# Optimization experiments

Hardware: AMD Instinct MI355X
Metric: run time of the kernel (lower is better)

The kernel has to match this reference:

```python
import jax, jax.numpy as jnp
import numpy as np

L, D, H, HD = 2, 2048, 16, 128          # layers, hidden, heads, head_dim
E, K, F, FS = 8, 2, 1408, 5632           # experts, top_k, moe_inter, shared_inter
V, T = 32000, 2048                       # vocab, tokens
EPS = 1e-6
ROPE_BASE = 1000000.0


def _rms(x, w):
    return x * jax.lax.rsqrt(jnp.mean(x * x, axis=-1, keepdims=True) + EPS) * w


def _rope(x, cos, sin):
    half = x.shape[-1] // 2
    x1, x2 = x[..., :half], x[..., half:]
    return jnp.concatenate([x1 * cos - x2 * sin, x1 * sin + x2 * cos], axis=-1)


def setup_inputs() -> dict:
    key = jax.random.key(0)
    ks = jax.random.split(key, 18)
    s = 0.02
    f = lambda k, shp: jax.random.normal(k, shp, jnp.float32) * s
    return {
        "input_ids": jax.random.randint(ks[0], (T,), 0, V, dtype=jnp.int32),
        "positions": jnp.arange(T, dtype=jnp.int32),
        "embed": f(ks[1], (V, D)),
        "qw": f(ks[2], (L, D, H * HD)),
        "kw": f(ks[3], (L, D, H * HD)),
        "vw": f(ks[4], (L, D, H * HD)),
        "ow": f(ks[5], (L, H * HD, D)),
        "ln1": jnp.ones((L, D), jnp.float32),
        "ln2": jnp.ones((L, D), jnp.float32),
        "router_w": f(ks[6], (L, D, E)),
        "sgate_w": f(ks[7], (L, D)),
        "wg": f(ks[8], (L, E, D, F)),
        "wu": f(ks[9], (L, E, D, F)),
        "wd": f(ks[10], (L, E, F, D)),
        "swg": f(ks[11], (L, D, FS)),
        "swu": f(ks[12], (L, D, FS)),
        "swd": f(ks[13], (L, FS, D)),
        "final_ln": jnp.ones((D,), jnp.float32),
    }


def _attn(x, positions, qw_l, kw_l, vw_l, ow_l):
    q = (x @ qw_l).reshape(T, H, HD)
    k = (x @ kw_l).reshape(T, H, HD)
    v = (x @ vw_l).reshape(T, H, HD)
    half = HD // 2
    inv = 1.0 / (ROPE_BASE ** (jnp.arange(half, dtype=jnp.float32) / half))
    ang = positions.astype(jnp.float32)[:, None] * inv[None, :]  # [T, half]
    cos, sin = jnp.cos(ang)[:, None, :], jnp.sin(ang)[:, None, :]
    q = _rope(q, cos, sin)
    k = _rope(k, cos, sin)
    scores = jnp.einsum('thd,shd->hts', q, k) * (HD ** -0.5)  # [H, T, T]
    mask = positions[:, None] >= positions[None, :]  # causal
    scores = jnp.where(mask[None], scores, -1e30)
    p = jax.nn.softmax(scores, axis=-1)
    o = jnp.einsum('hts,shd->thd', p, v).reshape(T, H * HD)
    return o @ ow_l


def _moe(x, router_w_l, sgate_w_l, wg_l, wu_l, wd_l, swg_l, swu_l, swd_l):
    # shared expert + its sigmoid gate
    sh = (jax.nn.silu(x @ swg_l) * (x @ swu_l)) @ swd_l
    sgate = jax.nn.sigmoid(x @ sgate_w_l)[:, None]
    # router: softmax in float32, then top-k with prob renorm (norm_topk_prob)
    probs = jax.nn.softmax((x @ router_w_l).astype(jnp.float32), axis=-1)
    topv, topi = jax.lax.top_k(probs, K)
    topv = topv / jnp.sum(topv, axis=-1, keepdims=True)
    combine = jnp.sum(jax.nn.one_hot(topi, E, dtype=x.dtype) * topv[..., None].astype(x.dtype), axis=1)  # [T, E]
    # dense grouped expert FFN, combined by routing weights (scatter-add equivalent)
    g = jnp.einsum('td,edf->etf', x, wg_l)
    u = jnp.einsum('td,edf->etf', x, wu_l)
    y = jnp.einsum('etf,efd->etd', jax.nn.silu(g) * u, wd_l)
    moe_out = jnp.einsum('te,etd->td', combine, y)
    return (moe_out + sgate * sh) * (1.0 / K ** 0.5)


def reference(input_ids, positions, embed, qw, kw, vw, ow, ln1, ln2, router_w,
              sgate_w, wg, wu, wd, swg, swu, swd, final_ln):
    h = embed[input_ids]  # [T, D]
    residual = None
    for l in range(L):
        if residual is None:
            residual = h
            x = _rms(h, ln1[l])
        else:
            residual = h + residual
            x = _rms(residual, ln1[l])
        h = _attn(x, positions, qw[l], kw[l], vw[l], ow[l])
        residual = h + residual
        x = _rms(residual, ln2[l])
        h = _moe(x, router_w[l], sgate_w[l], wg[l], wu[l], wd[l], swg[l], swu[l], swd[l])
    residual = h + residual
    return _rms(residual, final_ln)
```

## Files before the change

### kernel.cpp

```cpp
#include <hip/hip_runtime.h>
#include <stdint.h>

#define TT 2048
#define DD 2048
#define HH 16
#define HDIM 128
#define NE 8
#define TOPK 2
#define FF 1408
#define FSS 5632
#define NL 2

typedef __bf16 bf16;
typedef __bf16 bf16x2 __attribute__((ext_vector_type(2)));
typedef __bf16 bf16x4 __attribute__((ext_vector_type(4)));
typedef __bf16 bf16x8 __attribute__((ext_vector_type(8)));
typedef float f32x4 __attribute__((ext_vector_type(4)));

__device__ __forceinline__ void split1(float f, bf16& h, bf16& l) {
  bf16 hb = (bf16)f;
  h = hb;
  l = (bf16)(f - (float)hb);
}

__device__ __forceinline__ void gload16(const void* g, void* l) {
  __builtin_amdgcn_global_load_lds((const __attribute__((address_space(1))) void*)g,
                                   (__attribute__((address_space(3))) void*)l, 16, 0, 0);
}

template<bool LO>
__launch_bounds__(256)
__global__ void k_wtrans(const float* __restrict__ W, bf16* __restrict__ Wh,
                         bf16* __restrict__ Wl, int Kd, int N)
{
  __shared__ float T[64][68];
  const size_t slab = (size_t)blockIdx.z * (size_t)Kd * (size_t)N;
  const float* Wp = W + slab;
  const int k0 = blockIdx.x * 64, n0 = blockIdx.y * 64;
  const int tid = threadIdx.x;
  const int rr = tid >> 2, c4 = (tid & 3) * 4;
  const float* src = Wp + (size_t)(k0 + rr) * N + n0 + c4;
#pragma unroll
  for (int j = 0; j < 4; ++j) {
    f32x4 v = *(const f32x4*)(src + j * 16);
    *(f32x4*)&T[rr][c4 + j * 16] = v;
  }
  __syncthreads();
  const int nn = tid >> 2, kk = (tid & 3) * 16;
  bf16x8 h0, h1, l0, l1;
#pragma unroll
  for (int j = 0; j < 8; ++j) {
    bf16 hb, lb;
    split1(T[kk + j][nn], hb, lb);
    h0[j] = hb; l0[j] = lb;
    split1(T[kk + 8 + j][nn], hb, lb);
    h1[j] = hb; l1[j] = lb;
  }
  size_t out = slab + (size_t)(n0 + nn) * Kd + k0 + kk;
  *(bf16x8*)&Wh[out] = h0;
  *(bf16x8*)&Wh[out + 8] = h1;
  if (LO) {
    *(bf16x8*)&Wl[out] = l0;
    *(bf16x8*)&Wl[out + 8] = l1;
  }
}

template<int BMT, int NT, bool EXPERT, bool GATHER, int OM>
__launch_bounds__(256, (BMT == 128 ? 3 : 4))
__global__ void k_gemmp(const bf16* __restrict__ Ah, const bf16* __restrict__ Al,
                        const bf16* __restrict__ Bh, const bf16* __restrict__ Bl,
                        void* __restrict__ C1, void* __restrict__ C2,
                        int M, int N, int Kd, int lda, int ldc,
                        const int* __restrict__ perm, const int* __restrict__ cnt,
                        const int* __restrict__ ofs)
{
  constexpr int PL = (NT == 3) ? 2 : 1;
  constexpr int ASUB = BMT / 16;
  constexpr int AISS = PL * ASUB;
  constexpr int BISS = PL * 8;
  constexpr int QPW = (AISS + BISS) / 4;
  constexpr int IF = BMT / 32;

  int m_count = M, row_base = 0;
  size_t boff = 0;
  if (EXPERT) {
    int e = blockIdx.z;
    m_count = cnt[e];
    if ((int)(blockIdx.x * BMT) >= m_count) return;
    row_base = ofs[e];
    boff = (size_t)e * (size_t)N * (size_t)Kd;
  }
  const int tid = threadIdx.x, lane = tid & 63, wid = tid >> 6;
  const int wm = (wid >> 1) * (BMT / 2), wn = (wid & 1) * 64;
  const int lr = lane & 15, g = lane >> 4;
  const int n0 = blockIdx.y * 128;
  const int m0 = blockIdx.x * BMT;

  __shared__ bf16 As[PL][BMT][32];
  __shared__ bf16 Bs[PL][128][32];

  const bf16* srcp[QPW];
#pragma unroll
  for (int j = 0; j < QPW; ++j) {
    int q = wid * QPW + j;
    int r16 = lane >> 2;
    int kc = (lane & 3) ^ ((lane >> 3) & 3);
    if (q < AISS) {
      int pl = q / ASUB, sub = q % ASUB;
      int r = sub * 16 + r16;
      int tok;
      if (EXPERT) {
        int lrow = m0 + r;
        if (lrow >= m_count) lrow = m_count - 1;
        tok = GATHER ? perm[row_base + lrow] : (row_base + lrow);
      } else {
        tok = m0 + r;
      }
      const bf16* base = (pl == 0) ? Ah : Al;
      srcp[j] = base + (size_t)tok * lda + kc * 8;
    } else {
      int qb = q - AISS;
      int pl = qb >> 3, sub = qb & 7;
      int nrow = sub * 16 + r16;
      const bf16* base = (pl == 0) ? Bh : Bl;
      srcp[j] = base + boff + (size_t)(n0 + nrow) * Kd + kc * 8;
    }
  }

  f32x4 acc[IF][4];
#pragma unroll
  for (int i = 0; i < IF; ++i)
#pragma unroll
    for (int j = 0; j < 4; ++j)
      acc[i][j] = (f32x4){0.f, 0.f, 0.f, 0.f};

  auto ISSUE = [&](int k0) {
#pragma unroll
    for (int j = 0; j < QPW; ++j) {
      int q = wid * QPW + j;
      bf16* dst;
      if (q < AISS) {
        int pl = q / ASUB, sub = q % ASUB;
        dst = &As[pl][sub * 16][0];
      } else {
        int qb = q - AISS;
        int pl = qb >> 3, sub = qb & 7;
        dst = &Bs[pl][sub * 16][0];
      }
      gload16(srcp[j] + k0, dst);
    }
  };

  const int gs = (g ^ ((lr >> 1) & 3)) * 8;
  const int NTk = Kd >> 5;
  ISSUE(0);
  for (int t = 0; t < NTk; ++t) {
    __syncthreads();
    bf16x8 bfr[4][PL], afr[IF][PL];
#pragma unroll
    for (int jj = 0; jj < 4; ++jj)
#pragma unroll
      for (int pl = 0; pl < PL; ++pl)
        bfr[jj][pl] = *(const bf16x8*)&Bs[pl][wn + jj * 16 + lr][gs];
#pragma unroll
    for (int i = 0; i < IF; ++i)
#pragma unroll
      for (int pl = 0; pl < PL; ++pl)
        afr[i][pl] = *(const bf16x8*)&As[pl][wm + i * 16 + lr][gs];
    __syncthreads();
    if (t + 1 < NTk) ISSUE((t + 1) << 5);
#pragma unroll
    for (int i = 0; i < IF; ++i)
#pragma unroll
      for (int jj = 0; jj < 4; ++jj) {
        f32x4 a2 = acc[i][jj];
        a2 = __builtin_amdgcn_mfma_f32_16x16x32_bf16(afr[i][0], bfr[jj][0], a2, 0, 0, 0);
        if (NT == 3) {
          a2 = __builtin_amdgcn_mfma_f32_16x16x32_bf16(afr[i][0], bfr[jj][1], a2, 0, 0, 0);
          a2 = __builtin_amdgcn_mfma_f32_16x16x32_bf16(afr[i][1], bfr[jj][0], a2, 0, 0, 0);
        }
        acc[i][jj] = a2;
      }
  }

  const int r0 = g * 4;
#pragma unroll
  for (int i = 0; i < IF; ++i) {
    int lrow0 = m0 + wm + i * 16 + r0;
#pragma unroll
    for (int j = 0; j < 4; ++j) {
      int col = n0 + wn + j * 16 + lr;
      if (OM == 4) {
        bf16x4 ph, pl;
#pragma unroll
        for (int r = 0; r < 4; ++r) { bf16 hb, lb; split1(acc[i][j][r], hb, lb); ph[r] = hb; pl[r] = lb; }
        *(bf16x4*)&((bf16*)C1)[(size_t)col * ldc + lrow0] = ph;
        *(bf16x4*)&((bf16*)C2)[(size_t)col * ldc + lrow0] = pl;
      } else {
#pragma unroll
        for (int r = 0; r < 4; ++r) {
          int lrow = lrow0 + r;
          if (EXPERT && lrow >= m_count) continue;
          size_t off = (size_t)(row_base + lrow) * ldc + col;
          if (OM == 1) {
            ((float*)C1)[off] = acc[i][j][r];
          } else {
            bf16 hb, lb; split1(acc[i][j][r], hb, lb);
            ((bf16*)C1)[off] = hb;
            ((bf16*)C2)[off] = lb;
          }
        }
      }
    }
  }
}

__launch_bounds__(256)
__global__ void k_attns(const bf16* __restrict__ Qh, const bf16* __restrict__ Ql,
                        const bf16* __restrict__ Kh, const bf16* __restrict__ Kl,
                        const bf16* __restrict__ Vh, const bf16* __restrict__ Vl,
                        bf16* __restrict__ Oh, bf16* __restrict__ Ol)
{
  const int tid = threadIdx.x;
  const int lane = tid & 63, wid = tid >> 6;
  const int head = blockIdx.y;
  const int qbase = (gridDim.x - 1 - blockIdx.x) * 16;
  const int lr = lane & 15, g = lane >> 4;

  __shared__ float o_l[4][16][132];
  __shared__ float m_l[4][16], l_l[4][16];
  bf16* plbase = (bf16*)&o_l[0][0][0];
  bf16 (*pl_h)[40] = (bf16(*)[40])(plbase + wid * 16 * 40);
  bf16 (*pl_l)[40] = (bf16(*)[40])(plbase + (4 + wid) * 16 * 40);

  bf16x8 qfh[4], qfl[4];
  {
    size_t qoff = (size_t)(qbase + lr) * DD + head * HDIM;
#pragma unroll
    for (int c = 0; c < 4; ++c) {
      qfh[c] = *(const bf16x8*)(Qh + qoff + c * 32 + g * 8);
      qfl[c] = *(const bf16x8*)(Ql + qoff + c * 32 + g * 8);
    }
  }

  f32x4 o[8];
#pragma unroll
  for (int d = 0; d < 8; ++d) o[d] = (f32x4){0.f, 0.f, 0.f, 0.f};
  float m_r = -1e30f, l_r = 0.f;

  const int qend = qbase + 16;
  for (int kb = wid * 32; kb < qend; kb += 128) {
    f32x4 s0 = {0.f,0.f,0.f,0.f}, s1 = {0.f,0.f,0.f,0.f};
    size_t k0off = (size_t)(kb + lr) * DD + head * HDIM;
    size_t k1off = k0off + (size_t)16 * DD;
#pragma unroll
    for (int c = 0; c < 4; ++c) {
      bf16x8 kh = *(const bf16x8*)(Kh + k0off + c * 32 + g * 8);
      bf16x8 kl = *(const bf16x8*)(Kl + k0off + c * 32 + g * 8);
      s0 = __builtin_amdgcn_mfma_f32_16x16x32_bf16(kh, qfh[c], s0, 0, 0, 0);
      s0 = __builtin_amdgcn_mfma_f32_16x16x32_bf16(kl, qfh[c], s0, 0, 0, 0);
      s0 = __builtin_amdgcn_mfma_f32_16x16x32_bf16(kh, qfl[c], s0, 0, 0, 0);
    }
#pragma unroll
    for (int c = 0; c < 4; ++c) {
      bf16x8 kh = *(const bf16x8*)(Kh + k1off + c * 32 + g * 8);
      bf16x8 kl = *(const bf16x8*)(Kl + k1off + c * 32 + g * 8);
      s1 = __builtin_amdgcn_mfma_f32_16x16x32_bf16(kh, qfh[c], s1, 0, 0, 0);
      s1 = __builtin_amdgcn_mfma_f32_16x16x32_bf16(kl, qfh[c], s1, 0, 0, 0);
      s1 = __builtin_amdgcn_mfma_f32_16x16x32_bf16(kh, qfl[c], s1, 0, 0, 0);
    }
    float p0[4], p1[4];
    float mloc = -1e30f;
    const int q = qbase + lr;
#pragma unroll
    for (int r = 0; r < 4; ++r) {
      int k0i = kb + g * 4 + r;
      float a0 = s0[r] * 0.08838834764831845f;
      float a1 = s1[r] * 0.08838834764831845f;
      if (k0i > q)      a0 = -1e30f;
      if (k0i + 16 > q) a1 = -1e30f;
      p0[r] = a0; p1[r] = a1;
      mloc = fmaxf(mloc, fmaxf(a0, a1));
    }
    mloc = fmaxf(mloc, __shfl_xor(mloc, 16, 64));
    mloc = fmaxf(mloc, __shfl_xor(mloc, 32, 64));
    float mn = fmaxf(m_r, mloc);
    float alpha = __expf(m_r - mn);
    m_r = mn;
    float ps = 0.f;
#pragma unroll
    for (int r = 0; r < 4; ++r) {
      p0[r] = __expf(p0[r] - mn);
      p1[r] = __expf(p1[r] - mn);
      ps += p0[r] + p1[r];
    }
    ps += __shfl_xor(ps, 16, 64);
    ps += __shfl_xor(ps, 32, 64);
    l_r = l_r * alpha + ps;
    float alr[4];
#pragma unroll
    for (int r = 0; r < 4; ++r) alr[r] = __shfl(alpha, g * 4 + r, 64);
#pragma unroll
    for (int d = 0; d < 8; ++d)
#pragma unroll
      for (int r = 0; r < 4; ++r) o[d][r] *= alr[r];
#pragma unroll
    for (int r = 0; r < 4; ++r) {
      bf16 hb, lb;
      split1(p0[r], hb, lb);
      pl_h[lr][g * 4 + r] = hb;
      pl_l[lr][g * 4 + r] = lb;
      split1(p1[r], hb, lb);
      pl_h[lr][16 + g * 4 + r] = hb;
      pl_l[lr][16 + g * 4 + r] = lb;
    }
    bf16x8 pah = *(const bf16x8*)&pl_h[lr][g * 8];
    bf16x8 pal = *(const bf16x8*)&pl_l[lr][g * 8];
#pragma unroll
    for (int d = 0; d < 8; ++d) {
      size_t voff = (size_t)(head * HDIM + d * 16 + lr) * TT + kb + g * 8;
      bf16x8 vfh = *(const bf16x8*)(Vh + voff);
      bf16x8 vfl = *(const bf16x8*)(Vl + voff);
      o[d] = __builtin_amdgcn_mfma_f32_16x16x32_bf16(pah, vfh, o[d], 0, 0, 0);
      o[d] = __builtin_amdgcn_mfma_f32_16x16x32_bf16(pah, vfl, o[d], 0, 0, 0);
      o[d] = __builtin_amdgcn_mfma_f32_16x16x32_bf16(pal, vfh, o[d], 0, 0, 0);
    }
  }

  __syncthreads();
  if (g == 0) {
    m_l[wid][lr] = m_r;
    l_l[wid][lr] = l_r;
  }
#pragma unroll
  for (int d = 0; d < 8; ++d)
#pragma unroll
    for (int r = 0; r < 4; ++r)
      o_l[wid][g * 4 + r][d * 16 + lr] = o[d][r];
  __syncthreads();

  const int row = tid >> 4;
  const int c0 = (tid & 15) * 8;
  float m0v = m_l[0][row], m1v = m_l[1][row], m2v = m_l[2][row], m3v = m_l[3][row];
  float ms = fmaxf(fmaxf(m0v, m1v), fmaxf(m2v, m3v));
  float s0v = __expf(m0v - ms), s1v = __expf(m1v - ms);
  float s2v = __expf(m2v - ms), s3v = __expf(m3v - ms);
  float lsum = l_l[0][row] * s0v + l_l[1][row] * s1v
             + l_l[2][row] * s2v + l_l[3][row] * s3v;
  float inv = 1.f / lsum;
  union { bf16 b[8]; uint4 u; } ph, pl;
#pragma unroll
  for (int j = 0; j < 8; ++j) {
    float v = o_l[0][row][c0 + j] * s0v + o_l[1][row][c0 + j] * s1v
            + o_l[2][row][c0 + j] * s2v + o_l[3][row][c0 + j] * s3v;
    bf16 hb, lb;
    split1(v * inv, hb, lb);
    ph.b[j] = hb; pl.b[j] = lb;
  }
  size_t oi = (size_t)(qbase + row) * DD + head * HDIM + c0;
  *(uint4*)(Oh + oi) = ph.u;
  *(uint4*)(Ol + oi) = pl.u;
}

__global__ void k_embed(const int* __restrict__ ids, const float* __restrict__ Em,
                        float* __restrict__ Hout)
{
  int t = blockIdx.x, tid = threadIdx.x;
  const float4* s = (const float4*)(Em + (size_t)ids[t] * DD);
  float4* dst = (float4*)(Hout + (size_t)t * DD);
  dst[tid] = s[tid];
  dst[tid + 256] = s[tid + 256];
}

template<bool ADDIN, bool WF32, bool FINAL>
__launch_bounds__(256)
__global__ void k_addrms(const float* __restrict__ Hin, float* __restrict__ Res,
                         const float* __restrict__ W,
                         bf16* __restrict__ Xh, bf16* __restrict__ Xl,
                         float* __restrict__ Xf)
{
  const int t = blockIdx.x, tid = threadIdx.x;
  const size_t base = (size_t)t * DD + tid * 8;
  float x[8];
  {
    const float4* hp = (const float4*)(Hin + base);
    float4 a = hp[0], b = hp[1];
    x[0]=a.x; x[1]=a.y; x[2]=a.z; x[3]=a.w;
    x[4]=b.x; x[5]=b.y; x[6]=b.z; x[7]=b.w;
    if (ADDIN) {
      const float4* rp = (const float4*)(Res + base);
      float4 c = rp[0], d = rp[1];
      x[0]+=c.x; x[1]+=c.y; x[2]+=c.z; x[3]+=c.w;
      x[4]+=d.x; x[5]+=d.y; x[6]+=d.z; x[7]+=d.w;
    }
  }
  {
    float4* rp = (float4*)(Res + base);
    rp[0] = make_float4(x[0], x[1], x[2], x[3]);
    rp[1] = make_float4(x[4], x[5], x[6], x[7]);
  }
  float ss = 0.f;
#pragma unroll
  for (int j = 0; j < 8; ++j) ss += x[j] * x[j];
#pragma unroll
  for (int off = 32; off; off >>= 1) ss += __shfl_xor(ss, off, 64);
  __shared__ float red[4];
  if ((tid & 63) == 0) red[tid >> 6] = ss;
  __syncthreads();
  float tot = red[0] + red[1] + red[2] + red[3];
  float sc = rsqrtf(tot * (1.0f / DD) + 1e-6f);
  float y[8];
#pragma unroll
  for (int j = 0; j < 8; ++j) y[j] = x[j] * sc * W[tid * 8 + j];
  if (!FINAL) {
    union { bf16 b[8]; uint4 u; } ph, pl;
#pragma unroll
    for (int j = 0; j < 8; ++j) { bf16 hb, lb; split1(y[j], hb, lb); ph.b[j] = hb; pl.b[j] = lb; }
    *(uint4*)(Xh + base) = ph.u;
    *(uint4*)(Xl + base) = pl.u;
  }
  if (WF32 || FINAL) {
    float4* xp = (float4*)(Xf + base);
    xp[0] = make_float4(y[0], y[1], y[2], y[3]);
    xp[1] = make_float4(y[4], y[5], y[6], y[7]);
  }
}

__global__ void k_rope2(bf16* __restrict__ Qh, bf16* __restrict__ Ql,
                        bf16* __restrict__ Kh, bf16* __restrict__ Kl,
                        const int* __restrict__ pos)
{
  int idx = blockIdx.x * 256 + threadIdx.x;
  int d = idx & 63;
  int h = (idx >> 6) & (HH - 1);
  int t = idx >> 10;
  if (t >= TT) return;
  double inv = pow(1.0e6, -(double)d / 64.0);
  double ang = (double)pos[t] * inv;
  double sd, cd;
  sincos(ang, &sd, &cd);
  float sn = (float)sd, cs = (float)cd;
  size_t base = (size_t)t * DD + h * HDIM + d;
  float q1 = (float)Qh[base] + (float)Ql[base];
  float q2 = (float)Qh[base + 64] + (float)Ql[base + 64];
  float qa = q1 * cs - q2 * sn, qb = q1 * sn + q2 * cs;
  bf16 hb, lb;
  split1(qa, hb, lb); Qh[base] = hb;      Ql[base] = lb;
  split1(qb, hb, lb); Qh[base + 64] = hb; Ql[base + 64] = lb;
  float k1 = (float)Kh[base] + (float)Kl[base];
  float k2 = (float)Kh[base + 64] + (float)Kl[base + 64];
  float ka = k1 * cs - k2 * sn, kb2 = k1 * sn + k2 * cs;
  split1(ka, hb, lb);  Kh[base] = hb;      Kl[base] = lb;
  split1(kb2, hb, lb); Kh[base + 64] = hb; Kl[base + 64] = lb;
}

__launch_bounds__(64)
__global__ void k_router(const float* __restrict__ Xf, const float* __restrict__ RW,
                         const float* __restrict__ SGW, int* __restrict__ eidx,
                         float* __restrict__ ew, float* __restrict__ sgate,
                         int* __restrict__ cnt)
{
  const int t = blockIdx.x, lane = threadIdx.x;
  const float* x = Xf + (size_t)t * DD;
  float acc[8] = {0,0,0,0,0,0,0,0};
  float sg = 0.f;
  for (int i = lane; i < DD; i += 64) {
    float xv = x[i];
    const float4* w = (const float4*)(RW + (size_t)i * NE);
    float4 w0 = w[0], w1 = w[1];
    acc[0] += xv * w0.x; acc[1] += xv * w0.y; acc[2] += xv * w0.z; acc[3] += xv * w0.w;
    acc[4] += xv * w1.x; acc[5] += xv * w1.y; acc[6] += xv * w1.z; acc[7] += xv * w1.w;
    sg += xv * SGW[i];
  }
#pragma unroll
  for (int off = 32; off; off >>= 1) {
#pragma unroll
    for (int e = 0; e < 8; ++e) acc[e] += __shfl_xor(acc[e], off, 64);
    sg += __shfl_xor(sg, off, 64);
  }
  if (lane == 0) {
    int i0 = 0; float v0 = acc[0];
    for (int e = 1; e < 8; ++e) if (acc[e] > v0) { v0 = acc[e]; i0 = e; }
    int i1 = -1; float v1 = -1e30f;
    for (int e = 0; e < 8; ++e) if (e != i0 && acc[e] > v1) { v1 = acc[e]; i1 = e; }
    float w0 = 1.f / (1.f + expf(v1 - v0));
    eidx[2*t] = i0; eidx[2*t+1] = i1;
    ew[2*t] = w0; ew[2*t+1] = 1.f - w0;
    sgate[t] = 1.f / (1.f + expf(-sg));
    atomicAdd(&cnt[i0], 1);
    atomicAdd(&cnt[i1], 1);
  }
}

__global__ void k_scan(const int* __restrict__ cnt, int* __restrict__ ofs)
{
  if (threadIdx.x == 0) {
    int s = 0;
    for (int e = 0; e < NE; ++e) { ofs[e] = s; s += cnt[e]; }
    ofs[NE] = s;
  }
}

__global__ void k_assign(const int* __restrict__ eidx, const int* __restrict__ ofs,
                         int* __restrict__ cursor, int* __restrict__ perm,
                         int* __restrict__ posof)
{
  int t = blockIdx.x * 256 + threadIdx.x;
  if (t >= TT) return;
#pragma unroll
  for (int j = 0; j < 2; ++j) {
    int e = eidx[2*t + j];
    int p = ofs[e] + atomicAdd(&cursor[e], 1);
    perm[p] = t;
    posof[2*t + j] = p;
  }
}

__global__ void k_silup(const float* __restrict__ G, const float* __restrict__ U,
                        bf16* __restrict__ H, bf16* __restrict__ L)
{
  int i = (blockIdx.x * 256 + threadIdx.x) * 4;
  float4 g = *(const float4*)(G + i);
  float4 u = *(const float4*)(U + i);
  float s[4];
  s[0] = g.x / (1.f + expf(-g.x)) * u.x;
  s[1] = g.y / (1.f + expf(-g.y)) * u.y;
  s[2] = g.z / (1.f + expf(-g.z)) * u.z;
  s[3] = g.w / (1.f + expf(-g.w)) * u.w;
  bf16x4 h, l;
#pragma unroll
  for (int j = 0; j < 4; ++j) { bf16 hb, lb; split1(s[j], hb, lb); h[j] = hb; l[j] = lb; }
  *(bf16x4*)(H + i) = h;
  *(bf16x4*)(L + i) = l;
}

__global__ void k_combine(const float* __restrict__ Y, const float* __restrict__ SH,
                          const float* __restrict__ sgate, const float* __restrict__ ew,
                          const int* __restrict__ posof, float* __restrict__ Hout)
{
  int t = blockIdx.x, tid = threadIdx.x;
  int p0 = posof[2*t], p1 = posof[2*t+1];
  float w0 = ew[2*t], w1 = ew[2*t+1];
  float sgv = sgate[t];
  int d0 = tid * 8;
  const float4* a = (const float4*)(Y + (size_t)p0 * DD + d0);
  const float4* b = (const float4*)(Y + (size_t)p1 * DD + d0);
  float4 a0 = a[0], a1 = a[1], b0 = b[0], b1 = b[1];
  float y0[8] = {a0.x,a0.y,a0.z,a0.w,a1.x,a1.y,a1.z,a1.w};
  float y1[8] = {b0.x,b0.y,b0.z,b0.w,b1.x,b1.y,b1.z,b1.w};
  const float4* shp = (const float4*)(SH + (size_t)t * DD + d0);
  float4 sa = shp[0], sb = shp[1];
  float shv[8] = {sa.x, sa.y, sa.z, sa.w, sb.x, sb.y, sb.z, sb.w};
  float out[8];
#pragma unroll
  for (int j = 0; j < 8; ++j)
    out[j] = (y0[j] * w0 + y1[j] * w1 + sgv * shv[j]) * 0.70710678118654752f;
  float4* op = (float4*)(Hout + (size_t)t * DD + d0);
  op[0] = make_float4(out[0], out[1], out[2], out[3]);
  op[1] = make_float4(out[4], out[5], out[6], out[7]);
}

extern "C" void kernel_launch(void* const* d_in, const int* in_sizes, int n_in,
                              void* d_out, int out_size, void* d_ws, size_t ws_size,
                              hipStream_t stream)
{
  (void)in_sizes; (void)n_in; (void)out_size; (void)ws_size;
  const int*   ids  = (const int*)d_in[0];
  const int*   pos  = (const int*)d_in[1];
  const float* emb  = (const float*)d_in[2];
  const float* qw   = (const float*)d_in[3];
  const float* kw   = (const float*)d_in[4];
  const float* vw   = (const float*)d_in[5];
  const float* ow   = (const float*)d_in[6];
  const float* ln1  = (const float*)d_in[7];
  const float* ln2  = (const float*)d_in[8];
  const float* rw   = (const float*)d_in[9];
  const float* sgw  = (const float*)d_in[10];
  const float* wg   = (const float*)d_in[11];
  const float* wu   = (const float*)d_in[12];
  const float* wd   = (const float*)d_in[13];
  const float* swg  = (const float*)d_in[14];
  const float* swu  = (const float*)d_in[15];
  const float* swd  = (const float*)d_in[16];
  const float* fln  = (const float*)d_in[17];

  char* p = (char*)d_ws;
  auto alloc = [&](size_t b) { char* r = p; p += (b + 255) & ~(size_t)255; return r; };

  const size_t TD = (size_t)TT * DD;
  float* resid = (float*)alloc(TD * 4);
  float* hbuf  = (float*)alloc(TD * 4);
  float* xf    = (float*)alloc(TD * 4);
  bf16*  xh    = (bf16*) alloc(TD * 2);
  bf16*  xl    = (bf16*) alloc(TD * 2);
  bf16*  qhb   = (bf16*) alloc(TD * 2);
  bf16*  qlb   = (bf16*) alloc(TD * 2);
  bf16*  khb   = (bf16*) alloc(TD * 2);
  bf16*  klb   = (bf16*) alloc(TD * 2);
  bf16*  vth   = (bf16*) alloc(TD * 2);
  bf16*  vtl   = (bf16*) alloc(TD * 2);
  bf16*  aoh   = (bf16*) alloc(TD * 2);
  bf16*  aol   = (bf16*) alloc(TD * 2);
  float* shb   = (float*)alloc(TD * 4);
  const size_t SGF = (size_t)TT * FSS;
  const size_t GEF = (size_t)TT * TOPK * FF;
  bf16*  shph  = (bf16*) alloc(SGF * 2);
  bf16*  shpl  = (bf16*) alloc(SGF * 2);
  bf16*  geph  = (bf16*) alloc(GEF * 2);
  bf16*  gepl  = (bf16*) alloc(GEF * 2);
  float* region = (float*)alloc(2 * SGF * 4);
  float* sgbf = region;
  float* subf = region + SGF;
  float* gebf = region;
  float* uebf = region + GEF;
  float* ybf  = region + 2 * GEF;
  const size_t WME = (size_t)NE * DD * FF;
  bf16* wbh = (bf16*)alloc(WME * 2);
  bf16* wbl = (bf16*)alloc(WME * 2);
  int*   eidx  = (int*)  alloc((size_t)TT * TOPK * 4);
  float* ewb   = (float*)alloc((size_t)TT * TOPK * 4);
  float* sgate = (float*)alloc((size_t)TT * 4);
  int*   perm  = (int*)  alloc((size_t)TT * TOPK * 4);
  int*   posof = (int*)  alloc((size_t)TT * TOPK * 4);
  int*   cnt   = (int*)  alloc(64);
  int*   ofs   = (int*)  alloc(64);
  int*   cursor = cnt + 8;

  k_embed<<<TT, 256, 0, stream>>>(ids, emb, hbuf);

  for (int l = 0; l < NL; ++l) {
    const float* qw_l  = qw  + (size_t)l * DD * DD;
    const float* kw_l  = kw  + (size_t)l * DD * DD;
    const float* vw_l  = vw  + (size_t)l * DD * DD;
    const float* ow_l  = ow  + (size_t)l * DD * DD;
    const float* ln1_l = ln1 + (size_t)l * DD;
    const float* ln2_l = ln2 + (size_t)l * DD;
    const float* rw_l  = rw  + (size_t)l * DD * NE;
    const float* sgw_l = sgw + (size_t)l * DD;
    const float* wg_l  = wg  + (size_t)l * NE * DD * FF;
    const float* wu_l  = wu  + (size_t)l * NE * DD * FF;
    const float* wd_l  = wd  + (size_t)l * NE * FF * DD;
    const float* swg_l = swg + (size_t)l * DD * FSS;
    const float* swu_l = swu + (size_t)l * DD * FSS;
    const float* swd_l = swd + (size_t)l * FSS * DD;
    const bool last = (l == NL - 1);

    if (l == 0)
      k_addrms<false,false,false><<<TT,256,0,stream>>>(hbuf, resid, ln1_l, xh, xl, nullptr);
    else
      k_addrms<true, false,false><<<TT,256,0,stream>>>(hbuf, resid, ln1_l, xh, xl, nullptr);

    k_wtrans<true><<<dim3(32,32),256,0,stream>>>(qw_l, wbh, wbl, DD, DD);
    k_gemmp<64,3,false,false,3><<<dim3(32,16),256,0,stream>>>(xh, xl, wbh, wbl, qhb, qlb, TT, DD, DD, DD, DD, nullptr,nullptr,nullptr);
    k_wtrans<true><<<dim3(32,32),256,0,stream>>>(kw_l, wbh, wbl, DD, DD);
    k_gemmp<64,3,false,false,3><<<dim3(32,16),256,0,stream>>>(xh, xl, wbh, wbl, khb, klb, TT, DD, DD, DD, DD, nullptr,nullptr,nullptr);
    k_wtrans<true><<<dim3(32,32),256,0,stream>>>(vw_l, wbh, wbl, DD, DD);
    k_gemmp<64,3,false,false,4><<<dim3(32,16),256,0,stream>>>(xh, xl, wbh, wbl, vth, vtl, TT, DD, DD, DD, TT, nullptr,nullptr,nullptr);
    k_rope2<<<(TT*HH*64)/256, 256, 0, stream>>>(qhb, qlb, khb, klb, pos);
    k_attns<<<dim3(TT/16, HH), 256, 0, stream>>>(qhb, qlb, khb, klb, vth, vtl, aoh, aol);
    k_wtrans<true><<<dim3(32,32),256,0,stream>>>(ow_l, wbh, wbl, DD, DD);
    k_gemmp<64,3,false,false,1><<<dim3(32,16),256,0,stream>>>(aoh, aol, wbh, wbl, hbuf, nullptr, TT, DD, DD, DD, DD, nullptr,nullptr,nullptr);

    k_addrms<true,true,false><<<TT,256,0,stream>>>(hbuf, resid, ln2_l, xh, xl, xf);

    hipMemsetAsync(cnt, 0, 64, stream);
    k_router<<<TT, 64, 0, stream>>>(xf, rw_l, sgw_l, eidx, ewb, sgate, cnt);
    k_scan<<<1, 64, 0, stream>>>(cnt, ofs);
    k_assign<<<TT/256, 256, 0, stream>>>(eidx, ofs, cursor, perm, posof);

    if (!last) {
      k_wtrans<true><<<dim3(32,88),256,0,stream>>>(swg_l, wbh, wbl, DD, FSS);
      k_gemmp<128,3,false,false,1><<<dim3(16,44),256,0,stream>>>(xh, xl, wbh, wbl, sgbf, nullptr, TT, FSS, DD, DD, FSS, nullptr,nullptr,nullptr);
      k_wtrans<true><<<dim3(32,88),256,0,stream>>>(swu_l, wbh, wbl, DD, FSS);
      k_gemmp<128,3,false,false,1><<<dim3(16,44),256,0,stream>>>(xh, xl, wbh, wbl, subf, nullptr, TT, FSS, DD, DD, FSS, nullptr,nullptr,nullptr);
      k_silup<<<(TT*FSS/4)/256, 256, 0, stream>>>(sgbf, subf, shph, shpl);
      k_wtrans<true><<<dim3(88,32),256,0,stream>>>(swd_l, wbh, wbl, FSS, DD);
      k_gemmp<64,3,false,false,1><<<dim3(32,16),256,0,stream>>>(shph, shpl, wbh, wbl, shb, nullptr, TT, DD, FSS, FSS, DD, nullptr,nullptr,nullptr);
    } else {
      k_wtrans<false><<<dim3(32,88),256,0,stream>>>(swg_l, wbh, wbl, DD, FSS);
      k_gemmp<128,1,false,false,1><<<dim3(16,44),256,0,stream>>>(xh, xl, wbh, wbl, sgbf, nullptr, TT, FSS, DD, DD, FSS, nullptr,nullptr,nullptr);
      k_wtrans<false><<<dim3(32,88),256,0,stream>>>(swu_l, wbh, wbl, DD, FSS);
      k_gemmp<128,1,false,false,1><<<dim3(16,44),256,0,stream>>>(xh, xl, wbh, wbl, subf, nullptr, TT, FSS, DD, DD, FSS, nullptr,nullptr,nullptr);
      k_silup<<<(TT*FSS/4)/256, 256, 0, stream>>>(sgbf, subf, shph, shpl);
      k_wtrans<false><<<dim3(88,32),256,0,stream>>>(swd_l, wbh, wbl, FSS, DD);
      k_gemmp<64,1,false,false,1><<<dim3(32,16),256,0,stream>>>(shph, shpl, wbh, wbl, shb, nullptr, TT, DD, FSS, FSS, DD, nullptr,nullptr,nullptr);
    }

    if (!last) {
      k_wtrans<true><<<dim3(32,22,NE),256,0,stream>>>(wg_l, wbh, wbl, DD, FF);
      k_gemmp<64,3,true,true,1><<<dim3(64,11,NE),256,0,stream>>>(xh, xl, wbh, wbl, gebf, nullptr, TT, FF, DD, DD, FF, perm, cnt, ofs);
      k_wtrans<true><<<dim3(32,22,NE),256,0,stream>>>(wu_l, wbh, wbl, DD, FF);
      k_gemmp<64,3,true,true,1><<<dim3(64,11,NE),256,0,stream>>>(xh, xl, wbh, wbl, uebf, nullptr, TT, FF, DD, DD, FF, perm, cnt, ofs);
      k_silup<<<(GEF/4)/256, 256, 0, stream>>>(gebf, uebf, geph, gepl);
      k_wtrans<true><<<dim3(22,32,NE),256,0,stream>>>(wd_l, wbh, wbl, FF, DD);
      k_gemmp<64,3,true,false,1><<<dim3(64,16,NE),256,0,stream>>>(geph, gepl, wbh, wbl, ybf, nullptr, TT, DD, FF, FF, DD, nullptr, cnt, ofs);
    } else {
      k_wtrans<false><<<dim3(32,22,NE),256,0,stream>>>(wg_l, wbh, wbl, DD, FF);
      k_gemmp<64,1,true,true,1><<<dim3(64,11,NE),256,0,stream>>>(xh, xl, wbh, wbl, gebf, nullptr, TT, FF, DD, DD, FF, perm, cnt, ofs);
      k_wtrans<false><<<dim3(32,22,NE),256,0,stream>>>(wu_l, wbh, wbl, DD, FF);
      k_gemmp<64,1,true,true,1><<<dim3(64,11,NE),256,0,stream>>>(xh, xl, wbh, wbl, uebf, nullptr, TT, FF, DD, DD, FF, perm, cnt, ofs);
      k_silup<<<(GEF/4)/256, 256, 0, stream>>>(gebf, uebf, geph, gepl);
      k_wtrans<false><<<dim3(22,32,NE),256,0,stream>>>(wd_l, wbh, wbl, FF, DD);
      k_gemmp<64,1,true,false,1><<<dim3(64,16,NE),256,0,stream>>>(geph, gepl, wbh, wbl, ybf, nullptr, TT, DD, FF, FF, DD, nullptr, cnt, ofs);
    }
    k_combine<<<TT, 256, 0, stream>>>(ybf, shb, sgate, ewb, posof, hbuf);
  }

  k_addrms<true,false,true><<<TT,256,0,stream>>>(hbuf, resid, fln, nullptr, nullptr, (float*)d_out);
}
```

Measured before the change: 3.952 ms.

## Process two 16-row query tiles per attention block to reuse K/V loads

```diff
diff --git a/kernel.cpp b/kernel.cpp
--- a/kernel.cpp
+++ b/kernel.cpp
@@ -224,7 +224,7 @@
   const int tid = threadIdx.x;
   const int lane = tid & 63, wid = tid >> 6;
   const int head = blockIdx.y;
-  const int qbase = (gridDim.x - 1 - blockIdx.x) * 16;
+  const int qbase = (gridDim.x - 1 - blockIdx.x) * 32;
   const int lr = lane & 15, g = lane >> 4;
 
   __shared__ float o_l[4][16][132];
@@ -233,133 +233,233 @@
   bf16 (*pl_h)[40] = (bf16(*)[40])(plbase + wid * 16 * 40);
   bf16 (*pl_l)[40] = (bf16(*)[40])(plbase + (4 + wid) * 16 * 40);
 
-  bf16x8 qfh[4], qfl[4];
+  bf16x8 qfhA[4], qflA[4], qfhB[4], qflB[4];
   {
-    size_t qoff = (size_t)(qbase + lr) * DD + head * HDIM;
+    size_t qoffA = (size_t)(qbase + lr) * DD + head * HDIM;
+    size_t qoffB = qoffA + (size_t)16 * DD;
 #pragma unroll
     for (int c = 0; c < 4; ++c) {
-      qfh[c] = *(const bf16x8*)(Qh + qoff + c * 32 + g * 8);
-      qfl[c] = *(const bf16x8*)(Ql + qoff + c * 32 + g * 8);
-    }
-  }
-
-  f32x4 o[8];
-#pragma unroll
-  for (int d = 0; d < 8; ++d) o[d] = (f32x4){0.f, 0.f, 0.f, 0.f};
-  float m_r = -1e30f, l_r = 0.f;
-
-  const int qend = qbase + 16;
+      qfhA[c] = *(const bf16x8*)(Qh + qoffA + c * 32 + g * 8);
+      qflA[c] = *(const bf16x8*)(Ql + qoffA + c * 32 + g * 8);
+      qfhB[c] = *(const bf16x8*)(Qh + qoffB + c * 32 + g * 8);
+      qflB[c] = *(const bf16x8*)(Ql + qoffB + c * 32 + g * 8);
+    }
+  }
+
+  f32x4 oA[8], oB[8];
+#pragma unroll
+  for (int d = 0; d < 8; ++d) {
+    oA[d] = (f32x4){0.f, 0.f, 0.f, 0.f};
+    oB[d] = (f32x4){0.f, 0.f, 0.f, 0.f};
+  }
+  float mA = -1e30f, lA = 0.f;
+  float mB = -1e30f, lB = 0.f;
+
+  const int qend = qbase + 32;
   for (int kb = wid * 32; kb < qend; kb += 128) {
-    f32x4 s0 = {0.f,0.f,0.f,0.f}, s1 = {0.f,0.f,0.f,0.f};
+    f32x4 sA0 = {0.f,0.f,0.f,0.f}, sA1 = {0.f,0.f,0.f,0.f};
+    f32x4 sB0 = {0.f,0.f,0.f,0.f}, sB1 = {0.f,0.f,0.f,0.f};
     size_t k0off = (size_t)(kb + lr) * DD + head * HDIM;
     size_t k1off = k0off + (size_t)16 * DD;
 #pragma unroll
     for (int c = 0; c < 4; ++c) {
-      bf16x8 kh = *(const bf16x8*)(Kh + k0off + c * 32 + g * 8);
-      bf16x8 kl = *(const bf16x8*)(Kl + k0off + c * 32 + g * 8);
-      s0 = __builtin_amdgcn_mfma_f32_16x16x32_bf16(kh, qfh[c], s0, 0, 0, 0);
-      s0 = __builtin_amdgcn_mfma_f32_16x16x32_bf16(kl, qfh[c], s0, 0, 0, 0);
-      s0 = __builtin_amdgcn_mfma_f32_16x16x32_bf16(kh, qfl[c], s0, 0, 0, 0);
-    }
-#pragma unroll
-    for (int c = 0; c < 4; ++c) {
-      bf16x8 kh = *(const bf16x8*)(Kh + k1off + c * 32 + g * 8);
-      bf16x8 kl = *(const bf16x8*)(Kl + k1off + c * 32 + g * 8);
-      s1 = __builtin_amdgcn_mfma_f32_16x16x32_bf16(kh, qfh[c], s1, 0, 0, 0);
-      s1 = __builtin_amdgcn_mfma_f32_16x16x32_bf16(kl, qfh[c], s1, 0, 0, 0);
-      s1 = __builtin_amdgcn_mfma_f32_16x16x32_bf16(kh, qfl[c], s1, 0, 0, 0);
-    }
-    float p0[4], p1[4];
-    float mloc = -1e30f;
-    const int q = qbase + lr;
-#pragma unroll
-    for (int r = 0; r < 4; ++r) {
-      int k0i = kb + g * 4 + r;
-      float a0 = s0[r] * 0.08838834764831845f;
-      float a1 = s1[r] * 0.08838834764831845f;
-      if (k0i > q)      a0 = -1e30f;
-      if (k0i + 16 > q) a1 = -1e30f;
-      p0[r] = a0; p1[r] = a1;
-      mloc = fmaxf(mloc, fmaxf(a0, a1));
-    }
-    mloc = fmaxf(mloc, __shfl_xor(mloc, 16, 64));
-    mloc = fmaxf(mloc, __shfl_xor(mloc, 32, 64));
-    float mn = fmaxf(m_r, mloc);
-    float alpha = __expf(m_r - mn);
-    m_r = mn;
-    float ps = 0.f;
-#pragma unroll
-    for (int r = 0; r < 4; ++r) {
-      p0[r] = __expf(p0[r] - mn);
-      p1[r] = __expf(p1[r] - mn);
-      ps += p0[r] + p1[r];
-    }
-    ps += __shfl_xor(ps, 16, 64);
-    ps += __shfl_xor(ps, 32, 64);
-    l_r = l_r * alpha + ps;
-    float alr[4];
-#pragma unroll
-    for (int r = 0; r < 4; ++r) alr[r] = __shfl(alpha, g * 4 + r, 64);
-#pragma unroll
-    for (int d = 0; d < 8; ++d)
-#pragma unroll
-      for (int r = 0; r < 4; ++r) o[d][r] *= alr[r];
+      bf16x8 kh0 = *(const bf16x8*)(Kh + k0off + c * 32 + g * 8);
+      bf16x8 kl0 = *(const bf16x8*)(Kl + k0off + c * 32 + g * 8);
+      sA0 = __builtin_amdgcn_mfma_f32_16x16x32_bf16(kh0, qfhA[c], sA0, 0, 0, 0);
+      sA0 = __builtin_amdgcn_mfma_f32_16x16x32_bf16(kl0, qfhA[c], sA0, 0, 0, 0);
+      sA0 = __builtin_amdgcn_mfma_f32_16x16x32_bf16(kh0, qflA[c], sA0, 0, 0, 0);
+      sB0 = __builtin_amdgcn_mfma_f32_16x16x32_bf16(kh0, qfhB[c], sB0, 0, 0, 0);
+      sB0 = __builtin_amdgcn_mfma_f32_16x16x32_bf16(kl0, qfhB[c], sB0, 0, 0, 0);
+      sB0 = __builtin_amdgcn_mfma_f32_16x16x32_bf16(kh0, qflB[c], sB0, 0, 0, 0);
+      bf16x8 kh1 = *(const bf16x8*)(Kh + k1off + c * 32 + g * 8);
+      bf16x8 kl1 = *(const bf16x8*)(Kl + k1off + c * 32 + g * 8);
+      sA1 = __builtin_amdgcn_mfma_f32_16x16x32_bf16(kh1, qfhA[c], sA1, 0, 0, 0);
+      sA1 = __builtin_amdgcn_mfma_f32_16x16x32_bf16(kl1, qfhA[c], sA1, 0, 0, 0);
+      sA1 = __builtin_amdgcn_mfma_f32_16x16x32_bf16(kh1, qflA[c], sA1, 0, 0, 0);
+      sB1 = __builtin_amdgcn_mfma_f32_16x16x32_bf16(kh1, qfhB[c], sB1, 0, 0, 0);
+      sB1 = __builtin_amdgcn_mfma_f32_16x16x32_bf16(kl1, qfhB[c], sB1, 0, 0, 0);
+      sB1 = __builtin_amdgcn_mfma_f32_16x16x32_bf16(kh1, qflB[c], sB1, 0, 0, 0);
+    }
+    float p0A[4], p1A[4];
+    {
+      float mloc = -1e30f;
+      const int q = qbase + lr;
+#pragma unroll
+      for (int r = 0; r < 4; ++r) {
+        int k0i = kb + g * 4 + r;
+        float a0 = sA0[r] * 0.08838834764831845f;
+        float a1 = sA1[r] * 0.08838834764831845f;
+        if (k0i > q)      a0 = -1e30f;
+        if (k0i + 16 > q) a1 = -1e30f;
+        p0A[r] = a0; p1A[r] = a1;
+        mloc = fmaxf(mloc, fmaxf(a0, a1));
+      }
+      mloc = fmaxf(mloc, __shfl_xor(mloc, 16, 64));
+      mloc = fmaxf(mloc, __shfl_xor(mloc, 32, 64));
+      float mn = fmaxf(mA, mloc);
+      float alpha = __expf(mA - mn);
+      mA = mn;
+      float ps = 0.f;
+#pragma unroll
+      for (int r = 0; r < 4; ++r) {
+        p0A[r] = __expf(p0A[r] - mn);
+        p1A[r] = __expf(p1A[r] - mn);
+        ps += p0A[r] + p1A[r];
+      }
+      ps += __shfl_xor(ps, 16, 64);
+      ps += __shfl_xor(ps, 32, 64);
+      lA = lA * alpha + ps;
+      float alr[4];
+#pragma unroll
+      for (int r = 0; r < 4; ++r) alr[r] = __shfl(alpha, g * 4 + r, 64);
+#pragma unroll
+      for (int d = 0; d < 8; ++d)
+#pragma unroll
+        for (int r = 0; r < 4; ++r) oA[d][r] *= alr[r];
+    }
+    float p0B[4], p1B[4];
+    {
+      float mloc = -1e30f;
+      const int q = qbase + 16 + lr;
+#pragma unroll
+      for (int r = 0; r < 4; ++r) {
+        int k0i = kb + g * 4 + r;
+        float a0 = sB0[r] * 0.08838834764831845f;
+        float a1 = sB1[r] * 0.08838834764831845f;
+        if (k0i > q)      a0 = -1e30f;
+        if (k0i + 16 > q) a1 = -1e30f;
+        p0B[r] = a0; p1B[r] = a1;
+        mloc = fmaxf(mloc, fmaxf(a0, a1));
+      }
+      mloc = fmaxf(mloc, __shfl_xor(mloc, 16, 64));
+      mloc = fmaxf(mloc, __shfl_xor(mloc, 32, 64));
+      float mn = fmaxf(mB, mloc);
+      float alpha = __expf(mB - mn);
+      mB = mn;
+      float ps = 0.f;
+#pragma unroll
+      for (int r = 0; r < 4; ++r) {
+        p0B[r] = __expf(p0B[r] - mn);
+        p1B[r] = __expf(p1B[r] - mn);
+        ps += p0B[r] + p1B[r];
+      }
+      ps += __shfl_xor(ps, 16, 64);
+      ps += __shfl_xor(ps, 32, 64);
+      lB = lB * alpha + ps;
+      float alr[4];
+#pragma unroll
+      for (int r = 0; r < 4; ++r) alr[r] = __shfl(alpha, g * 4 + r, 64);
+#pragma unroll
+      for (int d = 0; d < 8; ++d)
+#pragma unroll
+        for (int r = 0; r < 4; ++r) oB[d][r] *= alr[r];
+    }
 #pragma unroll
     for (int r = 0; r < 4; ++r) {
       bf16 hb, lb;
-      split1(p0[r], hb, lb);
+      split1(p0A[r], hb, lb);
       pl_h[lr][g * 4 + r] = hb;
       pl_l[lr][g * 4 + r] = lb;
-      split1(p1[r], hb, lb);
+      split1(p1A[r], hb, lb);
       pl_h[lr][16 + g * 4 + r] = hb;
       pl_l[lr][16 + g * 4 + r] = lb;
     }
-    bf16x8 pah = *(const bf16x8*)&pl_h[lr][g * 8];
-    bf16x8 pal = *(const bf16x8*)&pl_l[lr][g * 8];
+    bf16x8 pahA = *(const bf16x8*)&pl_h[lr][g * 8];
+    bf16x8 palA = *(const bf16x8*)&pl_l[lr][g * 8];
+#pragma unroll
+    for (int r = 0; r < 4; ++r) {
+      bf16 hb, lb;
+      split1(p0B[r], hb, lb);
+      pl_h[lr][g * 4 + r] = hb;
+      pl_l[lr][g * 4 + r] = lb;
+      split1(p1B[r], hb, lb);
+      pl_h[lr][16 + g * 4 + r] = hb;
+      pl_l[lr][16 + g * 4 + r] = lb;
+    }
+    bf16x8 pahB = *(const bf16x8*)&pl_h[lr][g * 8];
+    bf16x8 palB = *(const bf16x8*)&pl_l[lr][g * 8];
 #pragma unroll
     for (int d = 0; d < 8; ++d) {
       size_t voff = (size_t)(head * HDIM + d * 16 + lr) * TT + kb + g * 8;
       bf16x8 vfh = *(const bf16x8*)(Vh + voff);
       bf16x8 vfl = *(const bf16x8*)(Vl + voff);
-      o[d] = __builtin_amdgcn_mfma_f32_16x16x32_bf16(pah, vfh, o[d], 0, 0, 0);
-      o[d] = __builtin_amdgcn_mfma_f32_16x16x32_bf16(pah, vfl, o[d], 0, 0, 0);
-      o[d] = __builtin_amdgcn_mfma_f32_16x16x32_bf16(pal, vfh, o[d], 0, 0, 0);
+      oA[d] = __builtin_amdgcn_mfma_f32_16x16x32_bf16(pahA, vfh, oA[d], 0, 0, 0);
+      oA[d] = __builtin_amdgcn_mfma_f32_16x16x32_bf16(pahA, vfl, oA[d], 0, 0, 0);
+      oA[d] = __builtin_amdgcn_mfma_f32_16x16x32_bf16(palA, vfh, oA[d], 0, 0, 0);
+      oB[d] = __builtin_amdgcn_mfma_f32_16x16x32_bf16(pahB, vfh, oB[d], 0, 0, 0);
+      oB[d] = __builtin_amdgcn_mfma_f32_16x16x32_bf16(pahB, vfl, oB[d], 0, 0, 0);
+      oB[d] = __builtin_amdgcn_mfma_f32_16x16x32_bf16(palB, vfh, oB[d], 0, 0, 0);
     }
   }
 
   __syncthreads();
   if (g == 0) {
-    m_l[wid][lr] = m_r;
-    l_l[wid][lr] = l_r;
+    m_l[wid][lr] = mA;
+    l_l[wid][lr] = lA;
   }
 #pragma unroll
   for (int d = 0; d < 8; ++d)
 #pragma unroll
     for (int r = 0; r < 4; ++r)
-      o_l[wid][g * 4 + r][d * 16 + lr] = o[d][r];
+      o_l[wid][g * 4 + r][d * 16 + lr] = oA[d][r];
   __syncthreads();
-
-  const int row = tid >> 4;
-  const int c0 = (tid & 15) * 8;
-  float m0v = m_l[0][row], m1v = m_l[1][row], m2v = m_l[2][row], m3v = m_l[3][row];
-  float ms = fmaxf(fmaxf(m0v, m1v), fmaxf(m2v, m3v));
-  float s0v = __expf(m0v - ms), s1v = __expf(m1v - ms);
-  float s2v = __expf(m2v - ms), s3v = __expf(m3v - ms);
-  float lsum = l_l[0][row] * s0v + l_l[1][row] * s1v
-             + l_l[2][row] * s2v + l_l[3][row] * s3v;
-  float inv = 1.f / lsum;
-  union { bf16 b[8]; uint4 u; } ph, pl;
-#pragma unroll
-  for (int j = 0; j < 8; ++j) {
-    float v = o_l[0][row][c0 + j] * s0v + o_l[1][row][c0 + j] * s1v
-            + o_l[2][row][c0 + j] * s2v + o_l[3][row][c0 + j] * s3v;
-    bf16 hb, lb;
-    split1(v * inv, hb, lb);
-    ph.b[j] = hb; pl.b[j] = lb;
-  }
-  size_t oi = (size_t)(qbase + row) * DD + head * HDIM + c0;
-  *(uint4*)(Oh + oi) = ph.u;
-  *(uint4*)(Ol + oi) = pl.u;
+  {
+    const int row = tid >> 4;
+    const int c0 = (tid & 15) * 8;
+    float m0v = m_l[0][row], m1v = m_l[1][row], m2v = m_l[2][row], m3v = m_l[3][row];
+    float ms = fmaxf(fmaxf(m0v, m1v), fmaxf(m2v, m3v));
+    float s0v = __expf(m0v - ms), s1v = __expf(m1v - ms);
+    float s2v = __expf(m2v - ms), s3v = __expf(m3v - ms);
+    float lsum = l_l[0][row] * s0v + l_l[1][row] * s1v
+               + l_l[2][row] * s2v + l_l[3][row] * s3v;
+    float inv = 1.f / lsum;
+    union { bf16 b[8]; uint4 u; } ph, pl;
+#pragma unroll
+    for (int j = 0; j < 8; ++j) {
+      float v = o_l[0][row][c0 + j] * s0v + o_l[1][row][c0 + j] * s1v
+              + o_l[2][row][c0 + j] * s2v + o_l[3][row][c0 + j] * s3v;
+      bf16 hb, lb;
+      split1(v * inv, hb, lb);
+      ph.b[j] = hb; pl.b[j] = lb;
+    }
+    size_t oi = (size_t)(qbase + row) * DD + head * HDIM + c0;
+    *(uint4*)(Oh + oi) = ph.u;
+    *(uint4*)(Ol + oi) = pl.u;
+  }
+  __syncthreads();
+  if (g == 0) {
+    m_l[wid][lr] = mB;
+    l_l[wid][lr] = lB;
+  }
+#pragma unroll
+  for (int d = 0; d < 8; ++d)
+#pragma unroll
+    for (int r = 0; r < 4; ++r)
+      o_l[wid][g * 4 + r][d * 16 + lr] = oB[d][r];
+  __syncthreads();
+  {
+    const int row = tid >> 4;
+    const int c0 = (tid & 15) * 8;
+    float m0v = m_l[0][row], m1v = m_l[1][row], m2v = m_l[2][row], m3v = m_l[3][row];
+    float ms = fmaxf(fmaxf(m0v, m1v), fmaxf(m2v, m3v));
+    float s0v = __expf(m0v - ms), s1v = __expf(m1v - ms);
+    float s2v = __expf(m2v - ms), s3v = __expf(m3v - ms);
+    float lsum = l_l[0][row] * s0v + l_l[1][row] * s1v
+               + l_l[2][row] * s2v + l_l[3][row] * s3v;
+    float inv = 1.f / lsum;
+    union { bf16 b[8]; uint4 u; } ph, pl;
+#pragma unroll
+    for (int j = 0; j < 8; ++j) {
+      float v = o_l[0][row][c0 + j] * s0v + o_l[1][row][c0 + j] * s1v
+              + o_l[2][row][c0 + j] * s2v + o_l[3][row][c0 + j] * s3v;
+      bf16 hb, lb;
+      split1(v * inv, hb, lb);
+      ph.b[j] = hb; pl.b[j] = lb;
+    }
+    size_t oi = (size_t)(qbase + 16 + row) * DD + head * HDIM + c0;
+    *(uint4*)(Oh + oi) = ph.u;
+    *(uint4*)(Ol + oi) = pl.u;
+  }
 }
 
 __global__ void k_embed(const int* __restrict__ ids, const float* __restrict__ Em,
@@ -657,7 +757,7 @@
     k_wtrans<true><<<dim3(32,32),256,0,stream>>>(vw_l, wbh, wbl, DD, DD);
     k_gemmp<64,3,false,false,4><<<dim3(32,16),256,0,stream>>>(xh, xl, wbh, wbl, vth, vtl, TT, DD, DD, DD, TT, nullptr,nullptr,nullptr);
     k_rope2<<<(TT*HH*64)/256, 256, 0, stream>>>(qhb, qlb, khb, klb, pos);
-    k_attns<<<dim3(TT/16, HH), 256, 0, stream>>>(qhb, qlb, khb, klb, vth, vtl, aoh, aol);
+    k_attns<<<dim3(TT/32, HH), 256, 0, stream>>>(qhb, qlb, khb, klb, vth, vtl, aoh, aol);
     k_wtrans<true><<<dim3(32,32),256,0,stream>>>(ow_l, wbh, wbl, DD, DD);
     k_gemmp<64,3,false,false,1><<<dim3(32,16),256,0,stream>>>(aoh, aol, wbh, wbl, hbuf, nullptr, TT, DD, DD, DD, DD, nullptr,nullptr,nullptr);
 
```

Result: faster. 3.710 ms (-6.1%).
